# Performance work log

Measured on AMD Instinct MI355X. Metric: run time of the kernel, lower is better.

## Reference

```python
import jax, jax.numpy as jnp
import numpy as np

B, T, C = 4, 2048, 1024
N_HEAD = 16
HEAD_DIM = C // N_HEAD


def setup_inputs() -> dict:
    key = jax.random.key(0)
    k1, k2, k3 = jax.random.split(key, 3)
    x = jax.random.normal(k1, (B, T, C), dtype=jnp.float32)
    w_attn = jax.random.normal(k2, (C, 3 * C), dtype=jnp.float32) * 0.02
    b_attn = jnp.zeros((3 * C,), dtype=jnp.float32)
    # c_proj init stddev = 0.02 / sqrt(2 * n_layer), n_layer = 24
    w_proj = jax.random.normal(k3, (C, C), dtype=jnp.float32) * (0.02 / np.sqrt(48.0))
    b_proj = jnp.zeros((C,), dtype=jnp.float32)
    return {"x": x, "w_attn": w_attn, "b_attn": b_attn,
            "w_proj": w_proj, "b_proj": b_proj}


def reference(x, w_attn, b_attn, w_proj, b_proj):
    Bx, Tx, Cx = x.shape
    scale = 1.0 / jnp.sqrt(jnp.asarray(HEAD_DIM, dtype=x.dtype))
    qkv = x @ w_attn + b_attn                      # [B,T,3C]
    qkv = qkv.reshape(Bx, Tx, 3, N_HEAD, HEAD_DIM)
    q, k, v = qkv[:, :, 0], qkv[:, :, 1], qkv[:, :, 2]  # each [B,T,H,D]
    att = jnp.einsum('bthd,bThd->bhtT', q, k) * scale   # [B,H,T,T]
    mask = jnp.tril(jnp.ones((Tx, Tx), dtype=x.dtype)).reshape(1, 1, Tx, Tx)
    att = att * mask - 1e10 * (1 - mask)
    att = jax.nn.softmax(att, axis=-1)
    y = jnp.einsum('bhtT,bThd->bthd', att, v)      # [B,T,H,D]
    y = y.reshape(Bx, Tx, Cx)
    return y @ w_proj + b_proj
```

## Files before the change

### kernel.cpp

```cpp
#include <hip/hip_runtime.h>
#include <hip/hip_bf16.h>


typedef __attribute__((ext_vector_type(8)))  __bf16 bf16x8;
typedef __attribute__((ext_vector_type(2)))  float  f32x2;
typedef __attribute__((ext_vector_type(4)))  float  f32x4;
typedef __attribute__((ext_vector_type(16))) float  f32x16;
typedef __attribute__((ext_vector_type(4)))  unsigned int u32x4;

#define AS1C(p) ((const __attribute__((address_space(1))) unsigned int*)(p))
#define AS3(p)  ((__attribute__((address_space(3))) unsigned int*)(p))

__device__ __forceinline__ unsigned short f2bfu(float f){
  __hip_bfloat16 h = __float2bfloat16(f);
  return __builtin_bit_cast(unsigned short, h);
}

__device__ __forceinline__ void plswapu(unsigned int &a, unsigned int &b){
  asm("v_permlane32_swap_b32 %0, %1" : "+v"(a), "+v"(b));
}
__device__ __forceinline__ unsigned int cvtpk(float lo, float hi){
  unsigned int r;
  asm("v_cvt_pk_bf16_f32 %0, %1, %2" : "=v"(r) : "v"(lo), "v"(hi));
  return r;
}
__device__ __forceinline__ float max3f(float a, float b, float c){
  float r;
  asm("v_max3_f32 %0, %1, %2, %3" : "=v"(r) : "v"(a), "v"(b), "v"(c));
  return r;
}


__global__ __launch_bounds__(256)
void f32_to_bf16_vec(const float* __restrict__ in, __hip_bfloat16* __restrict__ out, int n4){
  int stride = gridDim.x * blockDim.x;
  for (int i = blockIdx.x*blockDim.x + threadIdx.x; i < n4; i += stride){
    float4 v = reinterpret_cast<const float4*>(in)[i];
    ushort4 u;
    u.x = f2bfu(v.x); u.y = f2bfu(v.y); u.z = f2bfu(v.z); u.w = f2bfu(v.w);
    reinterpret_cast<ushort4*>(out)[i] = u;
  }
}

__global__ __launch_bounds__(256)
void transpose_to_bf16(const float* __restrict__ in, __hip_bfloat16* __restrict__ out, int R, int C){
  __shared__ float tile[32][33];
  const int tx = threadIdx.x & 31, ty = threadIdx.x >> 5;
  const int c0 = blockIdx.x*32, r0 = blockIdx.y*32;
  for (int i = ty; i < 32; i += 8)
    tile[i][tx] = in[(size_t)(r0+i)*C + c0 + tx];
  __syncthreads();
  for (int i = ty; i < 32; i += 8)
    out[(size_t)(c0+i)*R + r0 + tx] = __float2bfloat16(tile[tx][i]);
}


#define QSCALE 0.1803368801111244f

__device__ __forceinline__ void stage_ab(const __hip_bfloat16* __restrict__ A,
                                         const __hip_bfloat16* __restrict__ Bt,
                                         int m0, int n0, int K, int kt,
                                         __hip_bfloat16* sA, __hip_bfloat16* sB,
                                         int w, int l)
{
  const int k0 = kt*32;
  #pragma unroll
  for (int qq = 0; qq < 2; ++qq){
    const int c = qq*256 + w*64 + l;
    const int row = c>>2, kc = c&3;
    __builtin_amdgcn_global_load_lds(AS1C(A  + (size_t)(m0+row)*K + k0 + 8*kc),
                                     AS3(sA + (qq*256 + w*64)*8), 16, 0, 0);
    __builtin_amdgcn_global_load_lds(AS1C(Bt + (size_t)(n0+row)*K + k0 + 8*kc),
                                     AS3(sB + (qq*256 + w*64)*8), 16, 0, 0);
  }
}

template<int EPI>
__global__ __launch_bounds__(256)
void gemm_bf16(const __hip_bfloat16* __restrict__ A,
               const __hip_bfloat16* __restrict__ Bt,
               const float* __restrict__ bias,
               int M, int N, int K,
               __hip_bfloat16* __restrict__ q_s,
               __hip_bfloat16* __restrict__ k_s,
               __hip_bfloat16* __restrict__ vT_s,
               float* __restrict__ outf)
{
  __shared__ __align__(16) __hip_bfloat16 sA[2][128*32];
  __shared__ __align__(16) __hip_bfloat16 sB[2][128*32];
  const int tid = threadIdx.x, w = tid>>6, l = tid&63, g = l>>4, li = l&15;
  const int wm = w>>1, wn = w&1;

  const int nwg = gridDim.x, cpx = nwg >> 3;
  const int swz = (blockIdx.x & 7)*cpx + (blockIdx.x >> 3);
  const int nbx = N >> 7;
  const int m0 = (swz / nbx)*128, n0 = (swz % nbx)*128;

  f32x4 acc[4][4] = {};

  const int NT = K >> 5;
  stage_ab(A, Bt, m0, n0, K, 0, sA[0], sB[0], w, l);
  int cur = 0;

  for (int kt = 0; kt < NT; ++kt){
    __syncthreads();
    if (kt + 1 < NT)
      stage_ab(A, Bt, m0, n0, K, kt+1, sA[cur^1], sB[cur^1], w, l);

    bf16x8 af[4], bfr[4];
    #pragma unroll
    for (int mi = 0; mi < 4; ++mi)
      af[mi] = *reinterpret_cast<const bf16x8*>(sA[cur] + (wm*64 + mi*16 + li)*32 + 8*g);
    #pragma unroll
    for (int ni = 0; ni < 4; ++ni)
      bfr[ni] = *reinterpret_cast<const bf16x8*>(sB[cur] + (wn*64 + ni*16 + li)*32 + 8*g);
    #pragma unroll
    for (int mi = 0; mi < 4; ++mi)
      #pragma unroll
      for (int ni = 0; ni < 4; ++ni)
        acc[mi][ni] = __builtin_amdgcn_mfma_f32_16x16x32_bf16(af[mi], bfr[ni], acc[mi][ni], 0, 0, 0);
    cur ^= 1;
  }

  #pragma unroll
  for (int ni = 0; ni < 4; ++ni){
    const int col = n0 + wn*64 + ni*16 + li;
    const float bv = bias[col];
    #pragma unroll
    for (int mi = 0; mi < 4; ++mi){
      #pragma unroll
      for (int e = 0; e < 4; ++e){
        const int row = m0 + wm*64 + mi*16 + 4*g + e;
        const float val = acc[mi][ni][e] + bv;
        if (EPI == 0){
          const int three = col >> 10, h = (col >> 6) & 15, d = col & 63;
          const int b = row >> 11, t = row & 2047;
          const int bh = b*16 + h;
          if (three == 0)      q_s[((size_t)bh*2048 + t)*64 + d]  = __float2bfloat16(val*QSCALE);
          else if (three == 1) k_s[((size_t)bh*2048 + t)*64 + d]  = __float2bfloat16(val);
          else                 vT_s[((size_t)bh*64 + d)*2048 + t] = __float2bfloat16(val);
        } else {
          outf[(size_t)row*N + col] = val;
        }
      }
    }
  }
}


__device__ __forceinline__ void stage_kv(const __hip_bfloat16* __restrict__ k_s,
                                         const __hip_bfloat16* __restrict__ vT_s,
                                         size_t base, int j,
                                         __hip_bfloat16* sk, __hip_bfloat16* svt,
                                         int w, int l)
{
  #pragma unroll
  for (int qq = 0; qq < 2; ++qq){
    const int c = qq*256 + w*64 + l;
    const int r = c>>3, cc = c&7;
    __builtin_amdgcn_global_load_lds(AS1C(k_s  + base + (size_t)(j*64 + r)*64 + 8*(cc ^ (r&7))),
                                     AS3(sk  + (qq*256 + w*64)*8), 16, 0, 0);
    __builtin_amdgcn_global_load_lds(AS1C(vT_s + base + (size_t)r*2048 + j*64 + 8*(cc ^ (r&7))),
                                     AS3(svt + (qq*256 + w*64)*8), 16, 0, 0);
  }
}

__device__ __forceinline__ bf16x8 ldtile(const __hip_bfloat16* t, int row, int chunk){
  return *reinterpret_cast<const bf16x8*>(t + row*64 + ((chunk ^ (row&7))*8));
}

#define PFX(K) (((K)&1) ? pf2[(K)>>1].y : pf2[(K)>>1].x)

__device__ __forceinline__ void tile_compute(
    int j, int jd, int qabs, int h4, int lq, int h,
    const __hip_bfloat16* skc, const __hip_bfloat16* svtc,
    const bf16x8* qf,
    f32x16& o0, f32x16& o1, float& mrun, float& lrun)
{
  f32x16 s0 = {}, s1 = {};
  __builtin_amdgcn_s_setprio(1);
  #pragma unroll
  for (int ks = 0; ks < 4; ++ks){
    bf16x8 kf0 = ldtile(skc, lq,      2*ks + h);
    s0 = __builtin_amdgcn_mfma_f32_32x32x16_bf16(kf0, qf[ks], s0, 0, 0, 0);
    bf16x8 kf1 = ldtile(skc, 32 + lq, 2*ks + h);
    s1 = __builtin_amdgcn_mfma_f32_32x32x16_bf16(kf1, qf[ks], s1, 0, 0, 0);
  }
  __builtin_amdgcn_s_setprio(0);

  f32x2 pf2[16];
  #pragma unroll
  for (int i = 0; i < 8; ++i){
    pf2[i]     = (f32x2){ s0[2*i], s0[2*i+1] };
    pf2[8 + i] = (f32x2){ s1[2*i], s1[2*i+1] };
  }
  if (j == jd){
    const int rel = qabs - 64*j;
    #pragma unroll
    for (int i = 0; i < 16; ++i){
      const int a = i >> 3;
      const int r0 = (i & 7)*2, r1 = r0 + 1;
      const int kv0 = 32*a + (r0&3) + 8*(r0>>2) + h4;
      const int kv1 = 32*a + (r1&3) + 8*(r1>>2) + h4;
      pf2[i].x = (kv0 <= rel) ? pf2[i].x : -1e30f;
      pf2[i].y = (kv1 <= rel) ? pf2[i].y : -1e30f;
    }
  }

  float t0 = max3f(PFX(0),PFX(1),PFX(2)),   t1 = max3f(PFX(3),PFX(4),PFX(5));
  float t2 = max3f(PFX(6),PFX(7),PFX(8)),   t3 = max3f(PFX(9),PFX(10),PFX(11));
  float t4 = max3f(PFX(12),PFX(13),PFX(14)),t5 = max3f(PFX(15),PFX(16),PFX(17));
  float t6 = max3f(PFX(18),PFX(19),PFX(20)),t7 = max3f(PFX(21),PFX(22),PFX(23));
  float t8 = max3f(PFX(24),PFX(25),PFX(26)),t9 = max3f(PFX(27),PFX(28),PFX(29));
  float t10 = fmaxf(PFX(30),PFX(31));
  float u0 = max3f(t0,t1,t2), u1 = max3f(t3,t4,t5), u2 = max3f(t6,t7,t8);
  float u3 = fmaxf(t9,t10);
  float pm = fmaxf(max3f(u0,u1,u2), u3);

  if (!__all(pm - mrun <= 8.0f)){
    pm = fmaxf(pm, __shfl_xor(pm, 32));
    const float nm = fmaxf(mrun, pm);
    const float corr = exp2f(mrun - nm);
    mrun = nm;
    o0 *= corr; o1 *= corr;
    lrun *= corr;
  }

  const f32x2 negm = { -mrun, -mrun };
  #pragma unroll
  for (int i = 0; i < 16; ++i) pf2[i] = pf2[i] + negm;
  #pragma unroll
  for (int i = 0; i < 16; ++i){
    pf2[i].x = exp2f(pf2[i].x);
    pf2[i].y = exp2f(pf2[i].y);
  }

  f32x2 q8[8];
  #pragma unroll
  for (int i = 0; i < 8; ++i) q8[i] = pf2[i] + pf2[8+i];
  f32x2 q4a = q8[0]+q8[4], q4b = q8[1]+q8[5], q4c = q8[2]+q8[6], q4d = q8[3]+q8[7];
  f32x2 q2a = q4a+q4c, q2b = q4b+q4d;
  f32x2 q1 = q2a+q2b;
  float psum = q1.x + q1.y;
  psum += __shfl_xor(psum, 32);
  lrun += psum;

  unsigned int wds[16];
  #pragma unroll
  for (int k = 0; k < 16; ++k) wds[k] = cvtpk(pf2[k].x, pf2[k].y);
  #pragma unroll
  for (int a = 0; a < 2; ++a)
    #pragma unroll
    for (int bl = 0; bl < 2; ++bl){
      plswapu(wds[a*8 + 4*bl    ], wds[a*8 + 4*bl + 2]);
      plswapu(wds[a*8 + 4*bl + 1], wds[a*8 + 4*bl + 3]);
    }
  bf16x8 pfr[4];
  #pragma unroll
  for (int B = 0; B < 4; ++B){
    u32x4 t = { wds[4*B], wds[4*B+1], wds[4*B+2], wds[4*B+3] };
    pfr[B] = __builtin_bit_cast(bf16x8, t);
  }

  __builtin_amdgcn_s_setprio(1);
  #pragma unroll
  for (int ks = 0; ks < 4; ++ks){
    bf16x8 vf0 = ldtile(svtc, lq,      2*ks + h);
    o0 = __builtin_amdgcn_mfma_f32_32x32x16_bf16(vf0, pfr[ks], o0, 0, 0, 0);
    bf16x8 vf1 = ldtile(svtc, 32 + lq, 2*ks + h);
    o1 = __builtin_amdgcn_mfma_f32_32x32x16_bf16(vf1, pfr[ks], o1, 0, 0, 0);
  }
  __builtin_amdgcn_s_setprio(0);
}

__global__ __launch_bounds__(256)
void flash_attn(const __hip_bfloat16* __restrict__ q_s,
                const __hip_bfloat16* __restrict__ k_s,
                const __hip_bfloat16* __restrict__ vT_s,
                __hip_bfloat16* __restrict__ y_s)
{
  __shared__ __align__(16) __hip_bfloat16 sk [4][64*64];
  __shared__ __align__(16) __hip_bfloat16 svt[4][64*64];

  const int tid = threadIdx.x, w = tid>>6, l = tid&63;
  const int lq = l&31, h = l>>5, h4 = 4*h;
  const int bid = blockIdx.x;
  const int xcd = bid & 7, sl = (bid>>3) & 7, p = bid >> 6;
  const int bh = xcd*8 + sl;
  const size_t base = (size_t)bh * (2048*64);
  const int b = bh >> 4, hh = bh & 15;

  #pragma unroll 1
  for (int half = 0; half < 2; ++half){
    const int qbt = half ? p : (15 - p);
    const int q0w = qbt*128 + w*32;
    const int Jmax = 2*qbt + 1;
    const int jd = q0w >> 6;
    const int qabs = q0w + lq;

    bf16x8 qf[4];
    #pragma unroll
    for (int ks = 0; ks < 4; ++ks)
      qf[ks] = *reinterpret_cast<const bf16x8*>(q_s + base + (size_t)qabs*64 + 16*ks + 8*h);

    f32x16 o0 = {}, o1 = {};
    float mrun = -1e30f, lrun = 0.f;

    __syncthreads();
    stage_kv(k_s, vT_s, base, 0, sk[0], svt[0], w, l);
    stage_kv(k_s, vT_s, base, 1, sk[1], svt[1], w, l);

    #pragma unroll 1
    for (int jj = 0; jj <= Jmax; jj += 2){
      __syncthreads();
      if (jj + 2 <= Jmax)
        stage_kv(k_s, vT_s, base, jj+2, sk[(jj+2)&3], svt[(jj+2)&3], w, l);
      if (jj + 3 <= Jmax)
        stage_kv(k_s, vT_s, base, jj+3, sk[(jj+3)&3], svt[(jj+3)&3], w, l);

      if (jj <= jd)
        tile_compute(jj,   jd, qabs, h4, lq, h, sk[jj&3],     svt[jj&3],
                     qf, o0, o1, mrun, lrun);
      if (jj + 1 <= jd)
        tile_compute(jj+1, jd, qabs, h4, lq, h, sk[(jj+1)&3], svt[(jj+1)&3],
                     qf, o0, o1, mrun, lrun);
    }

    const float inv = 1.f / lrun;
    __hip_bfloat16* yp = y_s + ((size_t)(b*2048 + qabs))*1024 + hh*64;
    #pragma unroll
    for (int i = 0; i < 8; ++i){
      const int d = (2*i & 3) + 8*(i>>1) + h4;
      *reinterpret_cast<unsigned int*>(yp + d)      = cvtpk(o0[2*i]*inv, o0[2*i+1]*inv);
      *reinterpret_cast<unsigned int*>(yp + 32 + d) = cvtpk(o1[2*i]*inv, o1[2*i+1]*inv);
    }
  }
}


extern "C" void kernel_launch(void* const* d_in, const int* in_sizes, int n_in,
                              void* d_out, int out_size, void* d_ws, size_t ws_size,
                              hipStream_t stream)
{
  const float* x      = (const float*)d_in[0];
  const float* w_attn = (const float*)d_in[1];
  const float* b_attn = (const float*)d_in[2];
  const float* w_proj = (const float*)d_in[3];
  const float* b_proj = (const float*)d_in[4];
  float* out = (float*)d_out;
  char* ws = (char*)d_ws;

  __hip_bfloat16* xb     = (__hip_bfloat16*)(ws + 0);
  __hip_bfloat16* wattnT = (__hip_bfloat16*)(ws + 16777216);
  __hip_bfloat16* wprojT = (__hip_bfloat16*)(ws + 23068672);
  __hip_bfloat16* q_s    = (__hip_bfloat16*)(ws + 25165824);
  __hip_bfloat16* k_s    = (__hip_bfloat16*)(ws + 41943040);
  __hip_bfloat16* vT_s   = (__hip_bfloat16*)(ws + 58720256);
  __hip_bfloat16* y_s    = xb;

  f32_to_bf16_vec<<<2048, 256, 0, stream>>>(x, xb, 8388608/4);
  transpose_to_bf16<<<dim3(3072/32, 1024/32), 256, 0, stream>>>(w_attn, wattnT, 1024, 3072);
  transpose_to_bf16<<<dim3(1024/32, 1024/32), 256, 0, stream>>>(w_proj, wprojT, 1024, 1024);

  gemm_bf16<0><<<1536, 256, 0, stream>>>(
      xb, wattnT, b_attn, 8192, 3072, 1024, q_s, k_s, vT_s, (float*)nullptr);

  flash_attn<<<512, 256, 0, stream>>>(q_s, k_s, vT_s, y_s);

  gemm_bf16<1><<<512, 256, 0, stream>>>(
      y_s, wprojT, b_proj, 8192, 1024, 1024,
      (__hip_bfloat16*)nullptr, (__hip_bfloat16*)nullptr, (__hip_bfloat16*)nullptr, out);
}
```

Before: 213.7 us.

## Drop LDS staging in flash attention; load K/V directly from global per wave

Rewrites the attention kernel to load K and V^T fragments straight from global memory into registers instead of staging them through a swizzled, multi-buffered LDS ring with barriers. The grid becomes 2048 blocks of 128 threads, each handling 64 query rows, with no load-balancing pairing of query tiles. This removes the LDS traffic and block-wide syncs. In exchange, K/V tiles are no longer shared across waves in a block, so global/L2 traffic multiplies, the loads are not overlapped with compute, and the unpaired causal tiles leave work per block uneven.

```diff
diff --git a/kernel.cpp b/kernel.cpp
--- a/kernel.cpp
+++ b/kernel.cpp
@@ -148,192 +148,150 @@
 }
 
 
-__device__ __forceinline__ void stage_kv(const __hip_bfloat16* __restrict__ k_s,
-                                         const __hip_bfloat16* __restrict__ vT_s,
-                                         size_t base, int j,
-                                         __hip_bfloat16* sk, __hip_bfloat16* svt,
-                                         int w, int l)
-{
-  #pragma unroll
-  for (int qq = 0; qq < 2; ++qq){
-    const int c = qq*256 + w*64 + l;
-    const int r = c>>3, cc = c&7;
-    __builtin_amdgcn_global_load_lds(AS1C(k_s  + base + (size_t)(j*64 + r)*64 + 8*(cc ^ (r&7))),
-                                     AS3(sk  + (qq*256 + w*64)*8), 16, 0, 0);
-    __builtin_amdgcn_global_load_lds(AS1C(vT_s + base + (size_t)r*2048 + j*64 + 8*(cc ^ (r&7))),
-                                     AS3(svt + (qq*256 + w*64)*8), 16, 0, 0);
-  }
-}
-
-__device__ __forceinline__ bf16x8 ldtile(const __hip_bfloat16* t, int row, int chunk){
-  return *reinterpret_cast<const bf16x8*>(t + row*64 + ((chunk ^ (row&7))*8));
-}
-
-#define PFX(K) (((K)&1) ? pf2[(K)>>1].y : pf2[(K)>>1].x)
-
-__device__ __forceinline__ void tile_compute(
-    int j, int jd, int qabs, int h4, int lq, int h,
-    const __hip_bfloat16* skc, const __hip_bfloat16* svtc,
-    const bf16x8* qf,
-    f32x16& o0, f32x16& o1, float& mrun, float& lrun)
-{
-  f32x16 s0 = {}, s1 = {};
-  __builtin_amdgcn_s_setprio(1);
-  #pragma unroll
-  for (int ks = 0; ks < 4; ++ks){
-    bf16x8 kf0 = ldtile(skc, lq,      2*ks + h);
-    s0 = __builtin_amdgcn_mfma_f32_32x32x16_bf16(kf0, qf[ks], s0, 0, 0, 0);
-    bf16x8 kf1 = ldtile(skc, 32 + lq, 2*ks + h);
-    s1 = __builtin_amdgcn_mfma_f32_32x32x16_bf16(kf1, qf[ks], s1, 0, 0, 0);
-  }
-  __builtin_amdgcn_s_setprio(0);
-
-  f32x2 pf2[16];
-  #pragma unroll
-  for (int i = 0; i < 8; ++i){
-    pf2[i]     = (f32x2){ s0[2*i], s0[2*i+1] };
-    pf2[8 + i] = (f32x2){ s1[2*i], s1[2*i+1] };
-  }
-  if (j == jd){
-    const int rel = qabs - 64*j;
-    #pragma unroll
-    for (int i = 0; i < 16; ++i){
-      const int a = i >> 3;
-      const int r0 = (i & 7)*2, r1 = r0 + 1;
-      const int kv0 = 32*a + (r0&3) + 8*(r0>>2) + h4;
-      const int kv1 = 32*a + (r1&3) + 8*(r1>>2) + h4;
-      pf2[i].x = (kv0 <= rel) ? pf2[i].x : -1e30f;
-      pf2[i].y = (kv1 <= rel) ? pf2[i].y : -1e30f;
-    }
-  }
-
-  float t0 = max3f(PFX(0),PFX(1),PFX(2)),   t1 = max3f(PFX(3),PFX(4),PFX(5));
-  float t2 = max3f(PFX(6),PFX(7),PFX(8)),   t3 = max3f(PFX(9),PFX(10),PFX(11));
-  float t4 = max3f(PFX(12),PFX(13),PFX(14)),t5 = max3f(PFX(15),PFX(16),PFX(17));
-  float t6 = max3f(PFX(18),PFX(19),PFX(20)),t7 = max3f(PFX(21),PFX(22),PFX(23));
-  float t8 = max3f(PFX(24),PFX(25),PFX(26)),t9 = max3f(PFX(27),PFX(28),PFX(29));
-  float t10 = fmaxf(PFX(30),PFX(31));
-  float u0 = max3f(t0,t1,t2), u1 = max3f(t3,t4,t5), u2 = max3f(t6,t7,t8);
-  float u3 = fmaxf(t9,t10);
-  float pm = fmaxf(max3f(u0,u1,u2), u3);
-
-  if (!__all(pm - mrun <= 8.0f)){
-    pm = fmaxf(pm, __shfl_xor(pm, 32));
-    const float nm = fmaxf(mrun, pm);
-    const float corr = exp2f(mrun - nm);
-    mrun = nm;
-    o0 *= corr; o1 *= corr;
-    lrun *= corr;
-  }
-
-  const f32x2 negm = { -mrun, -mrun };
-  #pragma unroll
-  for (int i = 0; i < 16; ++i) pf2[i] = pf2[i] + negm;
-  #pragma unroll
-  for (int i = 0; i < 16; ++i){
-    pf2[i].x = exp2f(pf2[i].x);
-    pf2[i].y = exp2f(pf2[i].y);
-  }
-
-  f32x2 q8[8];
-  #pragma unroll
-  for (int i = 0; i < 8; ++i) q8[i] = pf2[i] + pf2[8+i];
-  f32x2 q4a = q8[0]+q8[4], q4b = q8[1]+q8[5], q4c = q8[2]+q8[6], q4d = q8[3]+q8[7];
-  f32x2 q2a = q4a+q4c, q2b = q4b+q4d;
-  f32x2 q1 = q2a+q2b;
-  float psum = q1.x + q1.y;
-  psum += __shfl_xor(psum, 32);
-  lrun += psum;
-
-  unsigned int wds[16];
-  #pragma unroll
-  for (int k = 0; k < 16; ++k) wds[k] = cvtpk(pf2[k].x, pf2[k].y);
-  #pragma unroll
-  for (int a = 0; a < 2; ++a)
-    #pragma unroll
-    for (int bl = 0; bl < 2; ++bl){
-      plswapu(wds[a*8 + 4*bl    ], wds[a*8 + 4*bl + 2]);
-      plswapu(wds[a*8 + 4*bl + 1], wds[a*8 + 4*bl + 3]);
-    }
-  bf16x8 pfr[4];
-  #pragma unroll
-  for (int B = 0; B < 4; ++B){
-    u32x4 t = { wds[4*B], wds[4*B+1], wds[4*B+2], wds[4*B+3] };
-    pfr[B] = __builtin_bit_cast(bf16x8, t);
-  }
-
-  __builtin_amdgcn_s_setprio(1);
-  #pragma unroll
-  for (int ks = 0; ks < 4; ++ks){
-    bf16x8 vf0 = ldtile(svtc, lq,      2*ks + h);
-    o0 = __builtin_amdgcn_mfma_f32_32x32x16_bf16(vf0, pfr[ks], o0, 0, 0, 0);
-    bf16x8 vf1 = ldtile(svtc, 32 + lq, 2*ks + h);
-    o1 = __builtin_amdgcn_mfma_f32_32x32x16_bf16(vf1, pfr[ks], o1, 0, 0, 0);
-  }
-  __builtin_amdgcn_s_setprio(0);
-}
-
-__global__ __launch_bounds__(256)
+__global__ __launch_bounds__(128, 4)
 void flash_attn(const __hip_bfloat16* __restrict__ q_s,
                 const __hip_bfloat16* __restrict__ k_s,
                 const __hip_bfloat16* __restrict__ vT_s,
                 __hip_bfloat16* __restrict__ y_s)
 {
-  __shared__ __align__(16) __hip_bfloat16 sk [4][64*64];
-  __shared__ __align__(16) __hip_bfloat16 svt[4][64*64];
-
   const int tid = threadIdx.x, w = tid>>6, l = tid&63;
   const int lq = l&31, h = l>>5, h4 = 4*h;
   const int bid = blockIdx.x;
-  const int xcd = bid & 7, sl = (bid>>3) & 7, p = bid >> 6;
+  const int xcd = bid & 7, sl = (bid>>3) & 7;
   const int bh = xcd*8 + sl;
+  const int qg = 31 - (bid >> 6);
   const size_t base = (size_t)bh * (2048*64);
   const int b = bh >> 4, hh = bh & 15;
 
-  #pragma unroll 1
-  for (int half = 0; half < 2; ++half){
-    const int qbt = half ? p : (15 - p);
-    const int q0w = qbt*128 + w*32;
-    const int Jmax = 2*qbt + 1;
-    const int jd = q0w >> 6;
-    const int qabs = q0w + lq;
-
-    bf16x8 qf[4];
-    #pragma unroll
-    for (int ks = 0; ks < 4; ++ks)
-      qf[ks] = *reinterpret_cast<const bf16x8*>(q_s + base + (size_t)qabs*64 + 16*ks + 8*h);
-
-    f32x16 o0 = {}, o1 = {};
-    float mrun = -1e30f, lrun = 0.f;
-
-    __syncthreads();
-    stage_kv(k_s, vT_s, base, 0, sk[0], svt[0], w, l);
-    stage_kv(k_s, vT_s, base, 1, sk[1], svt[1], w, l);
-
-    #pragma unroll 1
-    for (int jj = 0; jj <= Jmax; jj += 2){
-      __syncthreads();
-      if (jj + 2 <= Jmax)
-        stage_kv(k_s, vT_s, base, jj+2, sk[(jj+2)&3], svt[(jj+2)&3], w, l);
-      if (jj + 3 <= Jmax)
-        stage_kv(k_s, vT_s, base, jj+3, sk[(jj+3)&3], svt[(jj+3)&3], w, l);
-
-      if (jj <= jd)
-        tile_compute(jj,   jd, qabs, h4, lq, h, sk[jj&3],     svt[jj&3],
-                     qf, o0, o1, mrun, lrun);
-      if (jj + 1 <= jd)
-        tile_compute(jj+1, jd, qabs, h4, lq, h, sk[(jj+1)&3], svt[(jj+1)&3],
-                     qf, o0, o1, mrun, lrun);
-    }
-
-    const float inv = 1.f / lrun;
-    __hip_bfloat16* yp = y_s + ((size_t)(b*2048 + qabs))*1024 + hh*64;
+  const int q0w = qg*64 + w*32;
+  const int qabs = q0w + lq;
+
+  bf16x8 qf[4];
+  #pragma unroll
+  for (int ks = 0; ks < 4; ++ks)
+    qf[ks] = *reinterpret_cast<const bf16x8*>(q_s + base + (size_t)qabs*64 + 16*ks + 8*h);
+
+  f32x16 o0 = {}, o1 = {};
+  float mrun = -1e30f, lrun = 0.f;
+
+  for (int j = 0; j <= qg; ++j){
+    const __hip_bfloat16* kb = k_s  + base + (size_t)(j*64)*64;
+    const __hip_bfloat16* vb = vT_s + base + j*64;
+
+    bf16x8 kf0[4], kf1[4];
+    #pragma unroll
+    for (int ks = 0; ks < 4; ++ks){
+      kf0[ks] = *reinterpret_cast<const bf16x8*>(kb + (size_t)lq*64      + 16*ks + 8*h);
+      kf1[ks] = *reinterpret_cast<const bf16x8*>(kb + (size_t)(32+lq)*64 + 16*ks + 8*h);
+    }
+    f32x16 s0 = {}, s1 = {};
+    __builtin_amdgcn_s_setprio(1);
+    #pragma unroll
+    for (int ks = 0; ks < 4; ++ks){
+      s0 = __builtin_amdgcn_mfma_f32_32x32x16_bf16(kf0[ks], qf[ks], s0, 0, 0, 0);
+      s1 = __builtin_amdgcn_mfma_f32_32x32x16_bf16(kf1[ks], qf[ks], s1, 0, 0, 0);
+    }
+    __builtin_amdgcn_s_setprio(0);
+
+    bf16x8 vf0[4], vf1[4];
+    #pragma unroll
+    for (int ks = 0; ks < 4; ++ks){
+      vf0[ks] = *reinterpret_cast<const bf16x8*>(vb + (size_t)lq*2048      + 16*ks + 8*h);
+      vf1[ks] = *reinterpret_cast<const bf16x8*>(vb + (size_t)(32+lq)*2048 + 16*ks + 8*h);
+    }
+
+    f32x2 pf2[16];
     #pragma unroll
     for (int i = 0; i < 8; ++i){
-      const int d = (2*i & 3) + 8*(i>>1) + h4;
-      *reinterpret_cast<unsigned int*>(yp + d)      = cvtpk(o0[2*i]*inv, o0[2*i+1]*inv);
-      *reinterpret_cast<unsigned int*>(yp + 32 + d) = cvtpk(o1[2*i]*inv, o1[2*i+1]*inv);
-    }
+      pf2[i]     = (f32x2){ s0[2*i], s0[2*i+1] };
+      pf2[8 + i] = (f32x2){ s1[2*i], s1[2*i+1] };
+    }
+    if (j == qg){
+      const int rel = qabs - 64*j;
+      #pragma unroll
+      for (int i = 0; i < 16; ++i){
+        const int a = i >> 3;
+        const int r0 = (i & 7)*2, r1 = r0 + 1;
+        const int kv0 = 32*a + (r0&3) + 8*(r0>>2) + h4;
+        const int kv1 = 32*a + (r1&3) + 8*(r1>>2) + h4;
+        pf2[i].x = (kv0 <= rel) ? pf2[i].x : -1e30f;
+        pf2[i].y = (kv1 <= rel) ? pf2[i].y : -1e30f;
+      }
+    }
+
+    #define PFX(K) (((K)&1) ? pf2[(K)>>1].y : pf2[(K)>>1].x)
+    float t0 = max3f(PFX(0),PFX(1),PFX(2)),   t1 = max3f(PFX(3),PFX(4),PFX(5));
+    float t2 = max3f(PFX(6),PFX(7),PFX(8)),   t3 = max3f(PFX(9),PFX(10),PFX(11));
+    float t4 = max3f(PFX(12),PFX(13),PFX(14)),t5 = max3f(PFX(15),PFX(16),PFX(17));
+    float t6 = max3f(PFX(18),PFX(19),PFX(20)),t7 = max3f(PFX(21),PFX(22),PFX(23));
+    float t8 = max3f(PFX(24),PFX(25),PFX(26)),t9 = max3f(PFX(27),PFX(28),PFX(29));
+    float t10 = fmaxf(PFX(30),PFX(31));
+    float u0 = max3f(t0,t1,t2), u1 = max3f(t3,t4,t5), u2 = max3f(t6,t7,t8);
+    float u3 = fmaxf(t9,t10);
+    float pm = fmaxf(max3f(u0,u1,u2), u3);
+    #undef PFX
+
+    if (!__all(pm - mrun <= 8.0f)){
+      pm = fmaxf(pm, __shfl_xor(pm, 32));
+      const float nm = fmaxf(mrun, pm);
+      const float corr = exp2f(mrun - nm);
+      mrun = nm;
+      o0 *= corr; o1 *= corr;
+      lrun *= corr;
+    }
+
+    const f32x2 negm = { -mrun, -mrun };
+    #pragma unroll
+    for (int i = 0; i < 16; ++i) pf2[i] = pf2[i] + negm;
+    #pragma unroll
+    for (int i = 0; i < 16; ++i){
+      pf2[i].x = exp2f(pf2[i].x);
+      pf2[i].y = exp2f(pf2[i].y);
+    }
+
+    f32x2 q8[8];
+    #pragma unroll
+    for (int i = 0; i < 8; ++i) q8[i] = pf2[i] + pf2[8+i];
+    f32x2 q4a = q8[0]+q8[4], q4b = q8[1]+q8[5], q4c = q8[2]+q8[6], q4d = q8[3]+q8[7];
+    f32x2 q2a = q4a+q4c, q2b = q4b+q4d;
+    f32x2 q1 = q2a+q2b;
+    float psum = q1.x + q1.y;
+    psum += __shfl_xor(psum, 32);
+    lrun += psum;
+
+    unsigned int wds[16];
+    #pragma unroll
+    for (int k = 0; k < 16; ++k) wds[k] = cvtpk(pf2[k].x, pf2[k].y);
+    #pragma unroll
+    for (int a = 0; a < 2; ++a)
+      #pragma unroll
+      for (int bl = 0; bl < 2; ++bl){
+        plswapu(wds[a*8 + 4*bl    ], wds[a*8 + 4*bl + 2]);
+        plswapu(wds[a*8 + 4*bl + 1], wds[a*8 + 4*bl + 3]);
+      }
+    bf16x8 pfr[4];
+    #pragma unroll
+    for (int B = 0; B < 4; ++B){
+      u32x4 t = { wds[4*B], wds[4*B+1], wds[4*B+2], wds[4*B+3] };
+      pfr[B] = __builtin_bit_cast(bf16x8, t);
+    }
+
+    __builtin_amdgcn_s_setprio(1);
+    #pragma unroll
+    for (int ks = 0; ks < 4; ++ks){
+      o0 = __builtin_amdgcn_mfma_f32_32x32x16_bf16(vf0[ks], pfr[ks], o0, 0, 0, 0);
+      o1 = __builtin_amdgcn_mfma_f32_32x32x16_bf16(vf1[ks], pfr[ks], o1, 0, 0, 0);
+    }
+    __builtin_amdgcn_s_setprio(0);
+  }
+
+  const float inv = 1.f / lrun;
+  __hip_bfloat16* yp = y_s + ((size_t)(b*2048 + qabs))*1024 + hh*64;
+  #pragma unroll
+  for (int i = 0; i < 8; ++i){
+    const int d = (2*i & 3) + 8*(i>>1) + h4;
+    *reinterpret_cast<unsigned int*>(yp + d)      = cvtpk(o0[2*i]*inv, o0[2*i+1]*inv);
+    *reinterpret_cast<unsigned int*>(yp + 32 + d) = cvtpk(o1[2*i]*inv, o1[2*i+1]*inv);
   }
 }
 
@@ -365,7 +323,7 @@
   gemm_bf16<0><<<1536, 256, 0, stream>>>(
       xb, wattnT, b_attn, 8192, 3072, 1024, q_s, k_s, vT_s, (float*)nullptr);
 
-  flash_attn<<<512, 256, 0, stream>>>(q_s, k_s, vT_s, y_s);
+  flash_attn<<<2048, 128, 0, stream>>>(q_s, k_s, vT_s, y_s);
 
   gemm_bf16<1><<<512, 256, 0, stream>>>(
       y_s, wprojT, b_proj, 8192, 1024, 1024,
```

Measured after the change: 373.1 us. 1.75x slower.
